# Optimization experiments

Hardware: AMD Instinct MI355X
Metric: run time of the kernel (lower is better)

Reference implementation:

```python
import jax, jax.numpy as jnp
import numpy as np


def _made_masks(D, H):
    # Standard MADE masks, natural ordering, param_count=2 (shift, log_scale).
    d_in = np.arange(1, D + 1)                      # input degrees 1..D
    d_h = (np.arange(H) % (D - 1)) + 1              # hidden degrees cycle 1..D-1
    d_out = np.tile(d_in, 2)                        # output degrees, 2 params per dim
    M1 = (d_h[None, :] >= d_in[:, None]).astype(np.float32)   # [D, H]
    M2 = (d_out[None, :] > d_h[:, None]).astype(np.float32)
    return jnp.asarray(M1), jnp.asarray(M2)


def setup_inputs() -> dict:
    key = jax.random.key(0)
    B, D, H = 4096, 1024, 4096
    k0, k1, k2 = jax.random.split(key, 3)
    z = jax.random.normal(k0, (B, D), dtype=jnp.float32)
    W1 = jax.random.normal(k1, (D, H), dtype=jnp.float32) * (1.0 / np.sqrt(D))
    b1 = jnp.zeros((H,), dtype=jnp.float32)
    # small init on output layer keeps exp(log_scale) well-conditioned
    W2 = jax.random.normal(k2, (H, 2 * D), dtype=jnp.float32) * (0.1 / np.sqrt(H))
    b2 = jnp.zeros((2 * D,), dtype=jnp.float32)
    permutation = jnp.arange(D, dtype=jnp.int32)
    return {"z": z, "W1": W1, "b1": b1, "W2": W2, "b2": b2, "permutation": permutation}


def reference(z, W1, b1, W2, b2, permutation):
    # IAR.forward_flow: permute -> MADE masked MLP -> split params -> affine transform -> inverse permute
    D = z.shape[1]
    H = W1.shape[1]
    M1, M2 = _made_masks(D, H)
    zp = z[:, permutation]                          # permute_data
    h = jax.nn.relu(zp @ (W1 * M1) + b1)            # [B, H]
    res = h @ (W2 * M2) + b2                        # [B, 2D]
    mu, log_s = res[:, :D], res[:, D:]              # res.split(dim_in, dim=1)
    x = zp * jnp.exp(log_s) + mu                    # affine transform, forward=True
    log_det = jnp.sum(log_s, axis=1)                # [B]
    inv = jnp.argsort(permutation)                  # inv_permute_data
    return x[:, inv], log_det
```

## Files before the change

kernel.cpp:

```cpp
#include <hip/hip_runtime.h>
#include <stdint.h>


typedef float   f32x4  __attribute__((ext_vector_type(4)));
typedef int     i32x4  __attribute__((ext_vector_type(4)));
typedef int     i32x8  __attribute__((ext_vector_type(8)));

__device__ __forceinline__ uint8_t f2fp8(float f) {
    int p = __builtin_amdgcn_cvt_pk_fp8_f32(f, 0.0f, 0, false);
    return (uint8_t)(p & 0xff);
}
__device__ __forceinline__ int8_t f2i8(float v, float s) {
    float q = rintf(v * s);
    q = fminf(fmaxf(q, -127.0f), 127.0f);
    return (int8_t)q;
}

#define GLD16(g, l)                                                          \
    __builtin_amdgcn_global_load_lds(                                        \
        (const __attribute__((address_space(1))) uint32_t*)(g),              \
        (__attribute__((address_space(3))) uint32_t*)(l), 16, 0, 0)

#define MFMA_MX(a, b, c)                                                     \
    __builtin_amdgcn_mfma_scale_f32_16x16x128_f8f6f4(                        \
        (a), (b), (c), 0, 0, 0, 0x7F7F7F7F, 0, 0x7F7F7F7F)

__global__ __launch_bounds__(256) void prep_k(
    const float* __restrict__ W1, int8_t* __restrict__ W1mT,
    const float* __restrict__ W2, uint8_t* __restrict__ W2mT,
    float* __restrict__ ws2p,
    const float* __restrict__ z, const int* __restrict__ perm,
    int8_t* __restrict__ zp, float* __restrict__ ld,
    int D, int H, int B) {
    const int bx  = blockIdx.x;
    const int tid = threadIdx.x;
    const int NB1 = (H / 64) * (D / 64);
    const int NB2 = (2 * D / 64) * (H / 64);

    if (bx < NB1) {
        __shared__ int8_t t[64][68];
        const int c0 = (bx % (H / 64)) * 64;
        const int r0 = (bx / (H / 64)) * 64;
        const int tx = tid & 63, ty = tid >> 6;

        const int fid = bx * 256 + tid;
        if (fid < B) ld[fid] = 0.0f;

        for (int rr = ty; rr < 64; rr += 4) {
            const int r = r0 + rr, c = c0 + tx;
            float v = W1[(size_t)r * H + c];
            t[rr][tx] = ((c % (D - 1)) >= r) ? f2i8(v, 1024.0f) : (int8_t)0;
        }
        __syncthreads();
#pragma unroll
        for (int pass = 0; pass < 2; pass++) {
            const int cc = pass * 32 + (tid >> 3);
            const int j0 = (tid & 7) * 8;
            union { int8_t b[8]; uint64_t q; } v;
#pragma unroll
            for (int j = 0; j < 8; j++) v.b[j] = t[j0 + j][cc];
            *(uint64_t*)&W1mT[(size_t)(c0 + cc) * D + r0 + j0] = v.q;
        }
    } else if (bx < NB1 + NB2) {
        __shared__ uint8_t t[64][68];
        const int idx = bx - NB1;
        const int c0 = (idx % (2 * D / 64)) * 64;
        const int r0 = (idx / (2 * D / 64)) * 64;
        const int tx = tid & 63, ty = tid >> 6;
        const bool second = (c0 >= D);
        const int cb = (c0 - D) >> 6;

        for (int rr = ty; rr < 64; rr += 4) {
            const int r = r0 + rr, c = c0 + tx;
            float v = W2[(size_t)r * 2 * D + c];
            bool keep = ((c % D) > (r % (D - 1)));
            t[rr][tx] = keep ? f2fp8(v * 256.0f) : (uint8_t)0;
            if (second) {
                float s = keep ? v : 0.0f;
#pragma unroll
                for (int o = 32; o > 0; o >>= 1) s += __shfl_down(s, o, 64);
                if (tx == 0) ws2p[(size_t)cb * H + r] = s;
            }
        }
        __syncthreads();
#pragma unroll
        for (int pass = 0; pass < 2; pass++) {
            const int cc = pass * 32 + (tid >> 3);
            const int j0 = (tid & 7) * 8;
            union { uint8_t b[8]; uint64_t q; } v;
#pragma unroll
            for (int j = 0; j < 8; j++) v.b[j] = t[j0 + j][cc];
            *(uint64_t*)&W2mT[(size_t)(c0 + cc) * H + r0 + j0] = v.q;
        }
    } else {
        const int bp = bx - NB1 - NB2;
        const int i0 = tid * 4;
        const int4 p4 = *(const int4*)(perm + i0);
#pragma unroll
        for (int rr = 0; rr < 2; rr++) {
            const int b = bp * 2 + rr;
            const float* zr = z + (size_t)b * D;
            union { int8_t b4[4]; uint32_t u; } q;
            q.b4[0] = f2i8(zr[p4.x], 32.0f);
            q.b4[1] = f2i8(zr[p4.y], 32.0f);
            q.b4[2] = f2i8(zr[p4.z], 32.0f);
            q.b4[3] = f2i8(zr[p4.w], 32.0f);
            *(uint32_t*)&zp[(size_t)b * D + i0] = q.u;
        }
    }
}

__global__ __launch_bounds__(256) void gemm1_k(
    const int8_t* __restrict__ A, const int8_t* __restrict__ Bt,
    const float* __restrict__ bias, const float* __restrict__ ws2p,
    uint8_t* __restrict__ Cout, float* __restrict__ ld,
    int M, int N, int K) {
    __shared__ __align__(16) int8_t Alds[128 * 128];
    __shared__ __align__(16) int8_t Blds[128 * 128];
    __shared__ float pdl[128];

    const int id   = blockIdx.x;
    const int xcd  = id & 7, s = id >> 3;
    const int mb   = s & 31;
    const int nb   = xcd * 4 + (s >> 5);
    const int m0   = mb * 128;
    const int n0   = nb * 128;

    const int tid  = threadIdx.x;
    const int lane = tid & 63;
    const int w    = tid >> 6;
    const int wm   = (w & 1) * 64;
    const int wn   = (w >> 1) * 64;
    const int quad = lane >> 4;
    const int l16  = lane & 15;

    i32x4 acc[4][4];
#pragma unroll
    for (int i = 0; i < 4; i++)
#pragma unroll
        for (int j = 0; j < 4; j++) acc[i][j] = (i32x4)0;

    const int8_t* Ag[4];
    const int8_t* Bg[4];
    int8_t *Al[4], *Bl[4];
#pragma unroll
    for (int k = 0; k < 4; k++) {
        const int c  = tid + k * 256;
        const int so = ((c & 7) ^ ((c >> 3) & 7)) * 16;
        Ag[k] = A + (size_t)(m0 + (c >> 3)) * K + so;
        Bg[k] = Bt + (size_t)(n0 + (c >> 3)) * K + so;
        Al[k] = &Alds[c * 16];
        Bl[k] = &Blds[c * 16];
    }

    const int sw   = l16 & 7;
    const int arow = (wm + l16) * 128;
    const int brow = (wn + l16) * 128;

    for (int kt = 0; kt < K; kt += 128) {
        __syncthreads();
#pragma unroll
        for (int k = 0; k < 4; k++) {
            GLD16(Ag[k] + kt, Al[k]);
            GLD16(Bg[k] + kt, Bl[k]);
        }
        __syncthreads();

#pragma unroll
        for (int kh = 0; kh < 2; kh++) {
            const int pc = ((kh * 4 + quad) ^ sw) * 16;
            i32x4 af[4], bfr[4];
#pragma unroll
            for (int mi = 0; mi < 4; mi++)
                af[mi] = *(const i32x4*)&Alds[arow + mi * 16 * 128 + pc];
#pragma unroll
            for (int ni = 0; ni < 4; ni++)
                bfr[ni] = *(const i32x4*)&Blds[brow + ni * 16 * 128 + pc];
#pragma unroll
            for (int mi = 0; mi < 4; mi++)
#pragma unroll
                for (int ni = 0; ni < 4; ni++)
                    acc[mi][ni] = __builtin_amdgcn_mfma_i32_16x16x64_i8(
                        af[mi], bfr[ni], acc[mi][ni], 0, 0, 0);
        }
    }

    const float inv = 1.0f / 32768.0f;
    float bv[4], wv[4];
#pragma unroll
    for (int ni = 0; ni < 4; ni++) {
        const int col = n0 + wn + ni * 16 + l16;
        bv[ni] = bias[col];
        float sv = 0.0f;
#pragma unroll
        for (int cb = 0; cb < 16; cb++) sv += ws2p[(size_t)cb * N + col];
        wv[ni] = sv;
    }
    float pd[4][4];
#pragma unroll
    for (int mi = 0; mi < 4; mi++)
#pragma unroll
        for (int r = 0; r < 4; r++) pd[mi][r] = 0.0f;

#pragma unroll
    for (int mi = 0; mi < 4; mi++) {
        const int row = m0 + wm + mi * 16 + quad * 4;
#pragma unroll
        for (int ni = 0; ni < 4; ni++) {
            const int col = n0 + wn + ni * 16 + l16;
#pragma unroll
            for (int r = 0; r < 4; r++) {
                float v = fmaxf((float)acc[mi][ni][r] * inv + bv[ni], 0.0f);
                pd[mi][r] += v * wv[ni];
                Cout[(size_t)(row + r) * N + col] = f2fp8(v);
            }
        }
    }

#pragma unroll
    for (int off = 1; off < 16; off <<= 1)
#pragma unroll
        for (int mi = 0; mi < 4; mi++)
#pragma unroll
            for (int r = 0; r < 4; r++)
                pd[mi][r] += __shfl_xor(pd[mi][r], off, 16);

    __syncthreads();
    if ((w >> 1) == 0 && l16 == 0)
#pragma unroll
        for (int mi = 0; mi < 4; mi++)
#pragma unroll
            for (int r = 0; r < 4; r++)
                pdl[wm + mi * 16 + quad * 4 + r] = pd[mi][r];
    __syncthreads();
    if ((w >> 1) == 1 && l16 == 0)
#pragma unroll
        for (int mi = 0; mi < 4; mi++)
#pragma unroll
            for (int r = 0; r < 4; r++)
                pdl[wm + mi * 16 + quad * 4 + r] += pd[mi][r];
    __syncthreads();
    if (tid < 128) atomicAdd(&ld[m0 + tid], pdl[tid]);
}

__global__ __launch_bounds__(256) void gemm2f_k(
    const uint8_t* __restrict__ A, const uint8_t* __restrict__ Bt,
    const float* __restrict__ b2, const int* __restrict__ perm,
    const float* __restrict__ z, const float* __restrict__ ld,
    float* __restrict__ out, int B, int D, int K) {
    __shared__ __align__(16) uint8_t Alds[64 * 128];
    __shared__ __align__(16) uint8_t Blds[256 * 128];
    __shared__ float red[4];

    const int id   = blockIdx.x;
    const int nb   = id & 7;
    const int s    = id >> 3;
    const int m0   = s * 64;
    const int n0   = nb * 128;

    const int tid  = threadIdx.x;
    const int lane = tid & 63;
    const int w    = tid >> 6;
    const int wm   = (w & 1) * 32;
    const int wn   = (w >> 1) * 64;
    const int quad = lane >> 4;
    const int l16  = lane & 15;

    f32x4 acc[2][8];
#pragma unroll
    for (int i = 0; i < 2; i++)
#pragma unroll
        for (int j = 0; j < 8; j++) acc[i][j] = (f32x4)0.0f;

    const uint8_t* Ag[2];
    uint8_t* Al[2];
#pragma unroll
    for (int k = 0; k < 2; k++) {
        const int c  = tid + k * 256;
        const int so = ((c & 7) ^ ((c >> 3) & 7)) * 16;
        Ag[k] = A + (size_t)(m0 + (c >> 3)) * K + so;
        Al[k] = &Alds[c * 16];
    }
    const uint8_t* Bg[8];
    uint8_t* Bl[8];
#pragma unroll
    for (int k = 0; k < 8; k++) {
        const int c  = tid + k * 256;
        const int r  = c >> 3;
        const int g  = (r < 128) ? (n0 + r) : (D + n0 + (r - 128));
        const int so = ((c & 7) ^ (r & 7)) * 16;
        Bg[k] = Bt + (size_t)g * K + so;
        Bl[k] = &Blds[c * 16];
    }

    const int sw   = l16 & 7;
    const int pc0  = ((quad * 2) ^ sw) * 16;
    const int pc1  = ((quad * 2 + 1) ^ sw) * 16;
    const int arow = (wm + l16) * 128;
    int brow[8];
#pragma unroll
    for (int ni = 0; ni < 8; ni++)
        brow[ni] = ((ni >> 2) * 128 + wn + (ni & 3) * 16 + l16) * 128;

    for (int kt = 0; kt < K; kt += 128) {
        __syncthreads();
#pragma unroll
        for (int k = 0; k < 2; k++) GLD16(Ag[k] + kt, Al[k]);
#pragma unroll
        for (int k = 0; k < 8; k++) GLD16(Bg[k] + kt, Bl[k]);
        __syncthreads();

        union AB { int4 h2[2]; i32x8 v; };
        i32x8 af[2], bfr[8];
#pragma unroll
        for (int mi = 0; mi < 2; mi++) {
            AB t;
            t.h2[0] = *(const int4*)&Alds[arow + mi * 16 * 128 + pc0];
            t.h2[1] = *(const int4*)&Alds[arow + mi * 16 * 128 + pc1];
            af[mi] = t.v;
        }
#pragma unroll
        for (int ni = 0; ni < 8; ni++) {
            AB t;
            t.h2[0] = *(const int4*)&Blds[brow[ni] + pc0];
            t.h2[1] = *(const int4*)&Blds[brow[ni] + pc1];
            bfr[ni] = t.v;
        }
#pragma unroll
        for (int mi = 0; mi < 2; mi++)
#pragma unroll
            for (int ni = 0; ni < 8; ni++)
                acc[mi][ni] = MFMA_MX(af[mi], bfr[ni], acc[mi][ni]);
    }

    const float inv = 1.0f / 256.0f;
    float bmu[4], bls[4];
    int   pcv[4];
#pragma unroll
    for (int ci = 0; ci < 4; ci++) {
        const int gc = n0 + wn + ci * 16 + l16;
        bmu[ci] = b2[gc];
        bls[ci] = b2[D + gc];
        pcv[ci] = perm[gc];
    }
#pragma unroll
    for (int mi = 0; mi < 2; mi++) {
        const int row0 = m0 + wm + mi * 16 + quad * 4;
#pragma unroll
        for (int ci = 0; ci < 4; ci++) {
#pragma unroll
            for (int r = 0; r < 4; r++) {
                const size_t idx = (size_t)(row0 + r) * D + pcv[ci];
                const float mu = acc[mi][ci][r] * inv + bmu[ci];
                float ls = acc[mi][ci + 4][r] * inv + bls[ci];
                ls = fminf(fmaxf(ls, -30.0f), 30.0f);
                out[idx] = z[idx] * expf(ls) + mu;
            }
        }
    }

    if (nb == 0) {
        float bs = 0.0f;
        for (int i = tid; i < D; i += 256) bs += b2[D + i];
#pragma unroll
        for (int o = 32; o > 0; o >>= 1) bs += __shfl_down(bs, o, 64);
        if ((tid & 63) == 0) red[tid >> 6] = bs;
        __syncthreads();
        if (tid < 64)
            out[(size_t)B * D + m0 + tid] =
                ld[m0 + tid] + red[0] + red[1] + red[2] + red[3];
    }
}

extern "C" void kernel_launch(void* const* d_in, const int* in_sizes, int n_in,
                              void* d_out, int out_size, void* d_ws, size_t ws_size,
                              hipStream_t stream) {
    const float* z    = (const float*)d_in[0];
    const float* W1   = (const float*)d_in[1];
    const float* b1   = (const float*)d_in[2];
    const float* W2   = (const float*)d_in[3];
    const float* b2   = (const float*)d_in[4];
    const int*   perm = (const int*)d_in[5];
    float* out = (float*)d_out;
    char*  ws  = (char*)d_ws;

    const int D = in_sizes[5];
    const int H = in_sizes[2];
    const int B = in_sizes[0] / D;

    const size_t off_h    = 0;
    const size_t off_W2mT = off_h    + (size_t)B * H;
    const size_t off_W1mT = off_W2mT + (size_t)2 * D * H;
    const size_t off_zp   = off_W1mT + (size_t)H * D;
    const size_t off_ws2  = off_zp   + (size_t)B * D;
    const size_t off_ld   = off_ws2  + (size_t)16 * H * 4;

    uint8_t* h    = (uint8_t*)(ws + off_h);
    uint8_t* W2mT = (uint8_t*)(ws + off_W2mT);
    int8_t*  W1mT = (int8_t*)(ws + off_W1mT);
    int8_t*  zp   = (int8_t*)(ws + off_zp);
    float*   ws2p = (float*)(ws + off_ws2);
    float*   ld   = (float*)(ws + off_ld);

    const int NB1 = (H / 64) * (D / 64);
    const int NB2 = (2 * D / 64) * (H / 64);
    const int NBP = B / 2;
    prep_k<<<NB1 + NB2 + NBP, 256, 0, stream>>>(
        W1, W1mT, W2, W2mT, ws2p, z, perm, zp, ld, D, H, B);

    gemm1_k<<<(H / 128) * (B / 128), 256, 0, stream>>>(
        zp, W1mT, b1, ws2p, h, ld, B, H, D);

    gemm2f_k<<<(D / 128) * (B / 64), 256, 0, stream>>>(
        h, W2mT, b2, perm, z, ld, out, B, D, H);
}
```

Baseline: 194.4 us.

## Double-buffer gemm2 LDS tiles and reshape block to 128x64-pair tiles

The second fused GEMM kernel now prefetches the next K-slice into a second LDS buffer while computing on the current one, replacing the two barriers per iteration with one. The block tile changes from 64 rows by 128 mu/logscale column pairs to 128 rows by 64 pairs, so each warp holds a 4x4 MFMA accumulator grid and the A and B loads per block are balanced. This aims to hide global-to-LDS latency and improve operand reuse. In exchange it doubles LDS use to 64KB, which may lower occupancy. The log-det write is widened to cover 128 rows.

```diff
diff --git a/kernel.cpp b/kernel.cpp
--- a/kernel.cpp
+++ b/kernel.cpp
@@ -248,111 +248,112 @@
     const float* __restrict__ b2, const int* __restrict__ perm,
     const float* __restrict__ z, const float* __restrict__ ld,
     float* __restrict__ out, int B, int D, int K) {
-    __shared__ __align__(16) uint8_t Alds[64 * 128];
-    __shared__ __align__(16) uint8_t Blds[256 * 128];
+    __shared__ __align__(16) uint8_t Alds[2][128 * 128];
+    __shared__ __align__(16) uint8_t Blds[2][128 * 128];
     __shared__ float red[4];
 
     const int id   = blockIdx.x;
-    const int nb   = id & 7;
-    const int s    = id >> 3;
-    const int m0   = s * 64;
-    const int n0   = nb * 128;
+    const int nb   = id & 15;
+    const int s    = id >> 4;
+    const int m0   = s * 128;
+    const int p0   = nb * 64;
 
     const int tid  = threadIdx.x;
     const int lane = tid & 63;
     const int w    = tid >> 6;
-    const int wm   = (w & 1) * 32;
-    const int wn   = (w >> 1) * 64;
+    const int wm   = (w & 1) * 64;
+    const int wp   = (w >> 1) * 32;
     const int quad = lane >> 4;
     const int l16  = lane & 15;
 
-    f32x4 acc[2][8];
-#pragma unroll
-    for (int i = 0; i < 2; i++)
-#pragma unroll
-        for (int j = 0; j < 8; j++) acc[i][j] = (f32x4)0.0f;
-
-    const uint8_t* Ag[2];
-    uint8_t* Al[2];
-#pragma unroll
-    for (int k = 0; k < 2; k++) {
-        const int c  = tid + k * 256;
-        const int so = ((c & 7) ^ ((c >> 3) & 7)) * 16;
-        Ag[k] = A + (size_t)(m0 + (c >> 3)) * K + so;
-        Al[k] = &Alds[c * 16];
-    }
-    const uint8_t* Bg[8];
-    uint8_t* Bl[8];
-#pragma unroll
-    for (int k = 0; k < 8; k++) {
+    f32x4 acc[4][4];
+#pragma unroll
+    for (int i = 0; i < 4; i++)
+#pragma unroll
+        for (int j = 0; j < 4; j++) acc[i][j] = (f32x4)0.0f;
+
+    const uint8_t* Ag[4];
+    const uint8_t* Bg[4];
+    int ldso[4];
+#pragma unroll
+    for (int k = 0; k < 4; k++) {
         const int c  = tid + k * 256;
         const int r  = c >> 3;
-        const int g  = (r < 128) ? (n0 + r) : (D + n0 + (r - 128));
         const int so = ((c & 7) ^ (r & 7)) * 16;
+        Ag[k] = A + (size_t)(m0 + r) * K + so;
+        const int g = (r < 64) ? (p0 + r) : (D + p0 + (r - 64));
         Bg[k] = Bt + (size_t)g * K + so;
-        Bl[k] = &Blds[c * 16];
+        ldso[k] = c * 16;
     }
 
     const int sw   = l16 & 7;
     const int pc0  = ((quad * 2) ^ sw) * 16;
     const int pc1  = ((quad * 2 + 1) ^ sw) * 16;
-    const int arow = (wm + l16) * 128;
-    int brow[8];
-#pragma unroll
-    for (int ni = 0; ni < 8; ni++)
-        brow[ni] = ((ni >> 2) * 128 + wn + (ni & 3) * 16 + l16) * 128;
-
+
+#pragma unroll
+    for (int k = 0; k < 4; k++) {
+        GLD16(Ag[k], &Alds[0][ldso[k]]);
+        GLD16(Bg[k], &Blds[0][ldso[k]]);
+    }
+    __syncthreads();
+
+    int cur = 0;
     for (int kt = 0; kt < K; kt += 128) {
-        __syncthreads();
-#pragma unroll
-        for (int k = 0; k < 2; k++) GLD16(Ag[k] + kt, Al[k]);
-#pragma unroll
-        for (int k = 0; k < 8; k++) GLD16(Bg[k] + kt, Bl[k]);
-        __syncthreads();
-
-        union AB { int4 h2[2]; i32x8 v; };
-        i32x8 af[2], bfr[8];
-#pragma unroll
-        for (int mi = 0; mi < 2; mi++) {
-            AB t;
-            t.h2[0] = *(const int4*)&Alds[arow + mi * 16 * 128 + pc0];
-            t.h2[1] = *(const int4*)&Alds[arow + mi * 16 * 128 + pc1];
+        const int nxt = cur ^ 1;
+        if (kt + 128 < K) {
+#pragma unroll
+            for (int k = 0; k < 4; k++) {
+                GLD16(Ag[k] + kt + 128, &Alds[nxt][ldso[k]]);
+                GLD16(Bg[k] + kt + 128, &Blds[nxt][ldso[k]]);
+            }
+        }
+        union ABu { int4 h2[2]; i32x8 v; };
+        i32x8 af[4], bfr[4];
+#pragma unroll
+        for (int mi = 0; mi < 4; mi++) {
+            ABu t;
+            const int ar = (wm + mi * 16 + l16) * 128;
+            t.h2[0] = *(const int4*)&Alds[cur][ar + pc0];
+            t.h2[1] = *(const int4*)&Alds[cur][ar + pc1];
             af[mi] = t.v;
         }
 #pragma unroll
-        for (int ni = 0; ni < 8; ni++) {
-            AB t;
-            t.h2[0] = *(const int4*)&Blds[brow[ni] + pc0];
-            t.h2[1] = *(const int4*)&Blds[brow[ni] + pc1];
+        for (int ni = 0; ni < 4; ni++) {
+            ABu t;
+            const int br = ((ni >> 1) * 64 + wp + (ni & 1) * 16 + l16) * 128;
+            t.h2[0] = *(const int4*)&Blds[cur][br + pc0];
+            t.h2[1] = *(const int4*)&Blds[cur][br + pc1];
             bfr[ni] = t.v;
         }
 #pragma unroll
-        for (int mi = 0; mi < 2; mi++)
-#pragma unroll
-            for (int ni = 0; ni < 8; ni++)
+        for (int mi = 0; mi < 4; mi++)
+#pragma unroll
+            for (int ni = 0; ni < 4; ni++)
                 acc[mi][ni] = MFMA_MX(af[mi], bfr[ni], acc[mi][ni]);
+        __syncthreads();
+        cur = nxt;
     }
 
     const float inv = 1.0f / 256.0f;
-    float bmu[4], bls[4];
-    int   pcv[4];
-#pragma unroll
-    for (int ci = 0; ci < 4; ci++) {
-        const int gc = n0 + wn + ci * 16 + l16;
+    float bmu[2], bls[2];
+    int   pcv[2];
+#pragma unroll
+    for (int ci = 0; ci < 2; ci++) {
+        const int gc = p0 + wp + ci * 16 + l16;
         bmu[ci] = b2[gc];
         bls[ci] = b2[D + gc];
         pcv[ci] = perm[gc];
     }
 #pragma unroll
-    for (int mi = 0; mi < 2; mi++) {
+    for (int mi = 0; mi < 4; mi++) {
         const int row0 = m0 + wm + mi * 16 + quad * 4;
 #pragma unroll
-        for (int ci = 0; ci < 4; ci++) {
+        for (int ci = 0; ci < 2; ci++) {
 #pragma unroll
             for (int r = 0; r < 4; r++) {
                 const size_t idx = (size_t)(row0 + r) * D + pcv[ci];
                 const float mu = acc[mi][ci][r] * inv + bmu[ci];
-                float ls = acc[mi][ci + 4][r] * inv + bls[ci];
+                float ls = acc[mi][ci + 2][r] * inv + bls[ci];
                 ls = fminf(fmaxf(ls, -30.0f), 30.0f);
                 out[idx] = z[idx] * expf(ls) + mu;
             }
@@ -366,7 +367,7 @@
         for (int o = 32; o > 0; o >>= 1) bs += __shfl_down(bs, o, 64);
         if ((tid & 63) == 0) red[tid >> 6] = bs;
         __syncthreads();
-        if (tid < 64)
+        if (tid < 128)
             out[(size_t)B * D + m0 + tid] =
                 ld[m0 + tid] + red[0] + red[1] + red[2] + red[3];
     }
@@ -411,6 +412,6 @@
     gemm1_k<<<(H / 128) * (B / 128), 256, 0, stream>>>(
         zp, W1mT, b1, ws2p, h, ld, B, H, D);
 
-    gemm2f_k<<<(D / 128) * (B / 64), 256, 0, stream>>>(
+    gemm2f_k<<<(D / 64) * (B / 128), 256, 0, stream>>>(
         h, W2mT, b2, perm, z, ld, out, B, D, H);
 }
```

Result: faster. 189.2 us (-2.7%).
